# Performance work log

Measured on AMD Instinct MI355X. Metric: run time of the kernel, lower is better.

## Reference

```python
import jax, jax.numpy as jnp
import numpy as np

B, T, N, E, F_IN = 2, 8, 4000, 40000, 32
H, C, HL, FH = 4, 64, 128, 128  # heads, gat_hidden, lstm_hidden, fusion_hidden


def setup_inputs() -> dict:
    key = jax.random.key(0)
    ks = jax.random.split(key, 14)
    def nrm(i, shape, s=0.05):
        return jax.random.normal(ks[i], shape, jnp.float32) * s
    return {
        "x_seq": jax.random.normal(ks[0], (B, T, N, F_IN), jnp.float32),
        "W1": nrm(2, (F_IN, H * C)), "a_src1": nrm(3, (H, C)), "a_dst1": nrm(4, (H, C)), "b1": jnp.zeros((C,), jnp.float32),
        "W2": nrm(5, (C, H * C)), "a_src2": nrm(6, (H, C)), "a_dst2": nrm(7, (H, C)), "b2": jnp.zeros((C,), jnp.float32),
        "W_ih": nrm(8, (4 * HL, C)), "W_hh": nrm(9, (4 * HL, HL)),
        "b_ih": jnp.zeros((4 * HL,), jnp.float32), "b_hh": jnp.zeros((4 * HL,), jnp.float32),
        "Wf": nrm(10, (HL + C, FH)), "bf": jnp.zeros((FH,), jnp.float32),
        "Wo": nrm(11, (FH, 1)), "bo": jnp.zeros((1,), jnp.float32),
        "edge_index": jax.random.randint(ks[1], (2, E), 0, N, jnp.int64)
                      if jax.config.read("jax_enable_x64") else jax.random.randint(ks[1], (2, E), 0, N, jnp.int32),
    }


def gat_conv(x, src, dst, n, W, a_src, a_dst, b):
    """PyG GATConv, concat=False (mean over heads), self-loops already in src/dst."""
    h = (x @ W).reshape(n, H, C)                      # [N,H,C]
    al_s = jnp.einsum('nhc,hc->nh', h, a_src)         # [N,H]
    al_d = jnp.einsum('nhc,hc->nh', h, a_dst)
    logits = jax.nn.leaky_relu(al_s[src] + al_d[dst], negative_slope=0.2)  # [E',H]
    m = jax.ops.segment_max(logits, dst, num_segments=n)
    e = jnp.exp(logits - m[dst])
    denom = jax.ops.segment_sum(e, dst, num_segments=n)
    alpha = e / denom[dst]                            # segment-softmax over incoming edges
    out = jax.ops.segment_sum(alpha[:, :, None] * h[src], dst, num_segments=n)  # [N,H,C]
    return out.mean(axis=1) + b                       # [N,C]


def reference(x_seq, W1, a_src1, a_dst1, b1, W2, a_src2, a_dst2, b2,
              W_ih, W_hh, b_ih, b_hh, Wf, bf, Wo, bo, edge_index):
    Bd, Td, Nd, Fd = x_seq.shape
    loop = jnp.arange(Nd, dtype=edge_index.dtype)     # add_self_loops=True
    src = jnp.concatenate([edge_index[0], loop])
    dst = jnp.concatenate([edge_index[1], loop])

    def gat2(x):
        g1 = jax.nn.relu(gat_conv(x, src, dst, Nd, W1, a_src1, a_dst1, b1))
        return jax.nn.relu(gat_conv(g1, src, dst, Nd, W2, a_src2, a_dst2, b2))

    # batched over all B*T graph instances at once
    g = jax.vmap(gat2)(x_seq.reshape(Bd * Td, Nd, Fd)).reshape(Bd, Td, Nd, C)

    # LSTM over time, batch = B*N nodes
    seq = g.transpose(1, 0, 2, 3).reshape(Td, Bd * Nd, C)
    h0 = jnp.zeros((Bd * Nd, HL), x_seq.dtype)

    def step(carry, xt):
        h, c = carry
        z = xt @ W_ih.T + b_ih + h @ W_hh.T + b_hh
        i, f, gg, o = jnp.split(z, 4, axis=-1)        # torch gate order i,f,g,o
        c = jax.nn.sigmoid(f) * c + jax.nn.sigmoid(i) * jnp.tanh(gg)
        h = jax.nn.sigmoid(o) * jnp.tanh(c)
        return (h, c), None

    (hT, _), _ = jax.lax.scan(step, (h0, h0), seq)
    lstm_last = hT.reshape(Bd, Nd, HL)
    fused = jax.nn.relu(jnp.concatenate([lstm_last, g[:, -1]], axis=-1) @ Wf + bf)
    return (fused @ Wo + bo)[..., 0]                  # [B, N]
```

## Files before the change

### kernel.cpp

```cpp
#include <hip/hip_runtime.h>
#include <math.h>

#define NN 4000
#define EE 40000
#define NE 44000
#define BB 2
#define TT 8
#define BT 16
#define HH 4
#define CC 64
#define HC 256
#define HLN 128
#define G4 512
#define FHN 128
#define PADU 136
#define PADC 196

typedef __attribute__((ext_vector_type(8))) short short8v;
typedef __attribute__((ext_vector_type(4))) float f32x4;

__device__ __forceinline__ float fexp2(float x){ return __builtin_amdgcn_exp2f(x); }
__device__ __forceinline__ float frcp(float x){ return __builtin_amdgcn_rcpf(x); }
__device__ __forceinline__ float fsig(float x){ return frcp(1.f + fexp2(x * -1.44269504f)); }
__device__ __forceinline__ float ftanh(float x){
  float xx = fminf(fmaxf(x, -10.f), 10.f);
  float e = fexp2(xx * 2.88539008f);
  return (e - 1.f) * frcp(e + 1.f);
}
__device__ __forceinline__ unsigned short bf16rne(float x){
  unsigned u = __float_as_uint(x);
  return (unsigned short)((u + 0x7FFFu + ((u>>16)&1u)) >> 16);
}
__device__ __forceinline__ float bf2f(unsigned short h){ return __uint_as_float(((unsigned)h)<<16); }
__device__ __forceinline__ unsigned pack2(unsigned short a, unsigned short b){
  return ((unsigned)b << 16) | (unsigned)a;
}

__global__ void k_count(const int* __restrict__ dst, int* __restrict__ cnt){
  int e = blockIdx.x*256+threadIdx.x;
  if (e >= NE) return;
  int d = (e < EE) ? dst[e] : (e - EE);
  atomicAdd(&cnt[d], 1);
}

__global__ __launch_bounds__(1024) void k_scan(const int* __restrict__ cnt, int* __restrict__ ptr){
  __shared__ int part[1024];
  const int n = NN;
  int t = threadIdx.x;
  int base = t*4;
  int loc[4]; int s = 0;
  #pragma unroll
  for (int i=0;i<4;i++){ int c = (base+i < n) ? cnt[base+i] : 0; loc[i] = s; s += c; }
  part[t] = s;
  __syncthreads();
  for (int off=1; off<1024; off<<=1){
    int add = (t >= off) ? part[t-off] : 0;
    __syncthreads();
    part[t] += add;
    __syncthreads();
  }
  int ebase = (t > 0) ? part[t-1] : 0;
  #pragma unroll
  for (int i=0;i<4;i++){ if (base+i < n) ptr[base+i] = ebase + loc[i]; }
  if (t == 1023) ptr[n] = part[1023];
}

__global__ void k_scatter(const int* __restrict__ dst, const int* __restrict__ ptr,
                          int* __restrict__ cur, int* __restrict__ idxa){
  int e = blockIdx.x*256+threadIdx.x;
  if (e >= NE) return;
  int d = (e < EE) ? dst[e] : (e - EE);
  int pos = atomicAdd(&cur[d], 1);
  idxa[ptr[d]+pos] = e;
}

__global__ void k_sortseg(const int* __restrict__ ptr, int* __restrict__ idxa,
                          const int* __restrict__ e0, int* __restrict__ srcs){
  int node = blockIdx.x*256+threadIdx.x;
  if (node >= NN) return;
  int p0 = ptr[node], p1 = ptr[node+1];
  for (int i=p0+1;i<p1;i++){
    int key = idxa[i]; int j = i-1;
    while (j >= p0 && idxa[j] > key){ idxa[j+1] = idxa[j]; j--; }
    idxa[j+1] = key;
  }
  for (int p=p0;p<p1;p++){
    int e = idxa[p];
    srcs[p] = (e < EE) ? e0[e] : (e - EE);
  }
}

__global__ void k_prep(int* __restrict__ cnt,
                       const float* __restrict__ W1, const float* __restrict__ as1, const float* __restrict__ ad1,
                       const float* __restrict__ W2, const float* __restrict__ as2, const float* __restrict__ ad2,
                       float* __restrict__ wt,
                       const float* __restrict__ Wih, const float* __restrict__ Whh,
                       unsigned short* __restrict__ wfh, unsigned short* __restrict__ wfl,
                       const float* __restrict__ Wf, float* __restrict__ WfT,
                       unsigned short* __restrict__ wb1h, unsigned short* __restrict__ wb1l,
                       unsigned short* __restrict__ wb2h, unsigned short* __restrict__ wb2l){
  int i = blockIdx.x*256 + threadIdx.x;
  if (i < 2*NN){ cnt[i] = 0; return; }
  i -= 2*NN;
  if (i < 768){
    if (i < 256){
      int sd = i >> 7, h = (i >> 5) & 3, k = i & 31;
      const float* a = sd ? ad1 : as1;
      float s = 0.f;
      for (int c=0;c<CC;c++) s = fmaf(W1[k*HC + h*CC + c], a[h*CC + c], s);
      wt[sd*128 + h*32 + k] = s;
    } else {
      int j = i - 256;
      int sd = j >> 8, h = (j >> 6) & 3, k = j & 63;
      const float* a = sd ? ad2 : as2;
      float s = 0.f;
      for (int c=0;c<CC;c++) s = fmaf(W2[k*HC + h*CC + c], a[h*CC + c], s);
      wt[256 + sd*256 + h*64 + k] = s;
    }
    return;
  }
  i -= 768;
  if (i < 12288){
    int lane = i & 63;
    int kc = (i >> 6) % 6;
    int wk = i / (64*6);
    int w = wk & 7, gg = wk >> 3;
    int n = gg*128 + w*16 + (lane & 15);
    int kbase = kc*32 + (lane >> 4)*8;
    #pragma unroll
    for (int j=0;j<8;j++){
      int k = kbase + j;
      float v = (k < 64) ? Wih[n*64 + k] : Whh[n*128 + (k-64)];
      unsigned short hi = bf16rne(v);
      wfh[(size_t)i*8 + j] = hi;
      wfl[(size_t)i*8 + j] = bf16rne(v - bf2f(hi));
    }
    return;
  }
  i -= 12288;
  if (i < 24576){
    int u = i & 127, k = i >> 7;
    WfT[u*192 + k] = Wf[k*128 + u];
    return;
  }
  i -= 24576;
  if (i < 1024){
    int lane = i & 63, kc = (i >> 6) & 3, nt = i >> 8;
    int n = nt*16 + (lane & 15);
    int kb = kc*32 + (lane >> 4)*8;
    #pragma unroll
    for (int j=0;j<8;j++){
      int k = kb + j; int h = k >> 5; int kk = k & 31;
      float v = W1[kk*HC + h*CC + n];
      unsigned short hi = bf16rne(v);
      wb1h[(size_t)i*8 + j] = hi;
      wb1l[(size_t)i*8 + j] = bf16rne(v - bf2f(hi));
    }
    return;
  }
  i -= 1024;
  if (i < 2048){
    int lane = i & 63, kc = (i >> 6) & 7, nt = i >> 9;
    int n = nt*16 + (lane & 15);
    int kb = kc*32 + (lane >> 4)*8;
    #pragma unroll
    for (int j=0;j<8;j++){
      int k = kb + j; int h = k >> 6; int kk = k & 63;
      float v = W2[kk*HC + h*CC + n];
      unsigned short hi = bf16rne(v);
      wb2h[(size_t)i*8 + j] = hi;
      wb2l[(size_t)i*8 + j] = bf16rne(v - bf2f(hi));
    }
  }
}

template<int K>
__global__ void k_coef3(const float* __restrict__ x, const float* __restrict__ wts,
                        const float* __restrict__ wtd,
                        float* __restrict__ als, float* __restrict__ ald){
  int i = blockIdx.x*256+threadIdx.x;
  if (i >= BT*NN) return;
  const float* xp = x + (size_t)i*K;
  float s1[4] = {0.f,0.f,0.f,0.f};
  float s2[4] = {0.f,0.f,0.f,0.f};
  for (int k=0;k<K;k+=4){
    float4 xv = *(const float4*)&xp[k];
    #pragma unroll
    for (int h=0;h<4;h++){
      float4 sv = *(const float4*)&wts[h*K+k];
      float4 dv = *(const float4*)&wtd[h*K+k];
      s1[h] = fmaf(xv.x,sv.x,fmaf(xv.y,sv.y,fmaf(xv.z,sv.z,fmaf(xv.w,sv.w,s1[h]))));
      s2[h] = fmaf(xv.x,dv.x,fmaf(xv.y,dv.y,fmaf(xv.z,dv.z,fmaf(xv.w,dv.w,s2[h]))));
    }
  }
  *(float4*)&als[(size_t)i*4] = make_float4(s1[0],s1[1],s1[2],s1[3]);
  *(float4*)&ald[(size_t)i*4] = make_float4(s2[0],s2[1],s2[2],s2[3]);
}

template<int KF, bool SPLIT>
__global__ __launch_bounds__(256) void k_gatt(const int* __restrict__ ptr, const int* __restrict__ srcs,
    const float* __restrict__ als, const float* __restrict__ ald, const float* __restrict__ xin,
    const unsigned short* __restrict__ wbh, const unsigned short* __restrict__ wbl,
    const float* __restrict__ bias, float* __restrict__ outp,
    unsigned short* __restrict__ ohi, unsigned short* __restrict__ olo){
  constexpr int K = HH*KF;
  constexpr int PR = K + 8;
  constexpr int NKC = K/32;
  __shared__ float esh[16][64][HH];
  __shared__ float invs[16][HH];
  __shared__ unsigned short agh[16*PR];
  __shared__ unsigned short agl[16*PR];
  const int tid = threadIdx.x;
  const int lane = tid & 63;
  const int wv = tid >> 6;
  const int l15 = lane & 15;
  const int lg  = lane >> 4;
  const int bid = blockIdx.x;
  const int q = bid >> 3;
  const int hi2 = (q >= 250);
  const int inst = (bid & 7) + (hi2 ? 8 : 0);
  const int node0 = (hi2 ? q - 250 : q)*16;
  const size_t ibase = (size_t)inst*NN;
  {
    const int ns = lane >> 4;
    const int ei = lane & 15;
    const int nl = wv*4 + ns;
    const int node = node0 + nl;
    const int p0 = ptr[node], p1 = ptr[node+1];
    const float4 adv = *(const float4*)&ald[(ibase+node)*4];
    const float ad[4] = {adv.x, adv.y, adv.z, adv.w};
    float den[4] = {0.f,0.f,0.f,0.f};
    for (int p = p0 + ei; p < p1; p += 16){
      const int src = srcs[p];
      const float4 av = *(const float4*)&als[(ibase+src)*4];
      const float ac[4] = {av.x, av.y, av.z, av.w};
      float e4[4];
      #pragma unroll
      for (int h=0;h<4;h++){
        float v = ac[h] + ad[h];
        v = (v >= 0.f) ? v : 0.2f*v;
        float e = fexp2(v*1.44269504f);
        e4[h] = e;
        den[h] += e;
      }
      int slot = p - p0;
      if (slot < 64) *(float4*)&esh[nl][slot][0] = make_float4(e4[0],e4[1],e4[2],e4[3]);
    }
    #pragma unroll
    for (int h=0;h<4;h++){
      den[h] += __shfl_xor(den[h], 1);
      den[h] += __shfl_xor(den[h], 2);
      den[h] += __shfl_xor(den[h], 4);
      den[h] += __shfl_xor(den[h], 8);
    }
    if (ei == 0) *(float4*)&invs[nl][0] =
      make_float4(0.25f*frcp(den[0]), 0.25f*frcp(den[1]), 0.25f*frcp(den[2]), 0.25f*frcp(den[3]));
  }
  __syncthreads();
  constexpr int QL = KF/4;
  constexpr int EPAR = 64/QL;
  const int kq = lane & (QL-1);
  const int esub = lane / QL;
  for (int j=0;j<4;j++){
    const int nl = wv*4 + j;
    const int node = node0 + nl;
    const int p0 = ptr[node], p1 = ptr[node+1];
    float a[4][4];
    #pragma unroll
    for (int h=0;h<4;h++){ a[h][0]=0.f; a[h][1]=0.f; a[h][2]=0.f; a[h][3]=0.f; }
    for (int p = p0 + esub; p < p1; p += EPAR){
      const float4 ev = *(const float4*)&esh[nl][p - p0][0];
      const int src = srcs[p];
      const float4 xv = *(const float4*)&xin[(ibase + src)*(size_t)KF + kq*4];
      const float ec[4] = {ev.x, ev.y, ev.z, ev.w};
      const float xc[4] = {xv.x, xv.y, xv.z, xv.w};
      #pragma unroll
      for (int h=0;h<4;h++)
        #pragma unroll
        for (int c=0;c<4;c++)
          a[h][c] = fmaf(ec[h], xc[c], a[h][c]);
    }
    #pragma unroll
    for (int h=0;h<4;h++)
      #pragma unroll
      for (int c=0;c<4;c++){
        float v = a[h][c];
        if (EPAR == 8) v += __shfl_xor(v, 8);
        v += __shfl_xor(v, 16);
        v += __shfl_xor(v, 32);
        a[h][c] = v;
      }
    if (esub == 0){
      const float4 iv = *(const float4*)&invs[nl][0];
      const float ivc[4] = {iv.x, iv.y, iv.z, iv.w};
      #pragma unroll
      for (int h=0;h<4;h++){
        unsigned short vh[4], vl[4];
        #pragma unroll
        for (int c=0;c<4;c++){
          float v = a[h][c]*ivc[h];
          vh[c] = bf16rne(v);
          vl[c] = bf16rne(v - bf2f(vh[c]));
        }
        uint2 ph = {pack2(vh[0],vh[1]), pack2(vh[2],vh[3])};
        uint2 pl = {pack2(vl[0],vl[1]), pack2(vl[2],vl[3])};
        *(uint2*)&agh[nl*PR + h*KF + kq*4] = ph;
        *(uint2*)&agl[nl*PR + h*KF + kq*4] = pl;
      }
    }
  }
  __syncthreads();
  f32x4 acc = {0.f,0.f,0.f,0.f};
  #pragma unroll
  for (int kc=0; kc<NKC; kc++){
    size_t fl = (size_t)((wv*NKC + kc)*64 + lane)*8;
    short8v BH = *(const short8v*)&wbh[fl];
    short8v BL = *(const short8v*)&wbl[fl];
    int aoff = l15*PR + kc*32 + lg*8;
    short8v AH = *(const short8v*)&agh[aoff];
    short8v AL = *(const short8v*)&agl[aoff];
    acc = __builtin_amdgcn_mfma_f32_16x16x32_bf16(AH, BH, acc, 0,0,0);
    acc = __builtin_amdgcn_mfma_f32_16x16x32_bf16(AH, BL, acc, 0,0,0);
    acc = __builtin_amdgcn_mfma_f32_16x16x32_bf16(AL, BH, acc, 0,0,0);
  }
  const int c = wv*16 + l15;
  const float bv = bias[c];
  #pragma unroll
  for (int r=0;r<4;r++){
    int node = node0 + lg*4 + r;
    float val = fmaxf(acc[r] + bv, 0.f);
    size_t oi = (ibase + node)*CC + c;
    if constexpr (SPLIT){
      unsigned short hv = bf16rne(val);
      ohi[oi] = hv;
      olo[oi] = bf16rne(val - bf2f(hv));
    } else {
      outp[oi] = val;
    }
  }
}

__device__ __forceinline__ void mfma24(const short8v (&AH)[2], const short8v (&AL)[2],
                                       const short8v (&BH)[4], const short8v (&BL)[4],
                                       f32x4 (&acc)[2][4]){
  #pragma unroll
  for (int mt=0;mt<2;mt++)
    #pragma unroll
    for (int gg=0;gg<4;gg++)
      acc[mt][gg] = __builtin_amdgcn_mfma_f32_16x16x32_bf16(AH[mt], BH[gg], acc[mt][gg], 0,0,0);
  #pragma unroll
  for (int mt=0;mt<2;mt++)
    #pragma unroll
    for (int gg=0;gg<4;gg++)
      acc[mt][gg] = __builtin_amdgcn_mfma_f32_16x16x32_bf16(AH[mt], BL[gg], acc[mt][gg], 0,0,0);
  #pragma unroll
  for (int mt=0;mt<2;mt++)
    #pragma unroll
    for (int gg=0;gg<4;gg++)
      acc[mt][gg] = __builtin_amdgcn_mfma_f32_16x16x32_bf16(AL[mt], BH[gg], acc[mt][gg], 0,0,0);
}

__global__ __launch_bounds__(512) void k_lstm7(
    const unsigned short* __restrict__ ghi, const unsigned short* __restrict__ glo,
    const unsigned short* __restrict__ wfh, const unsigned short* __restrict__ wfl,
    const float* __restrict__ bih, const float* __restrict__ bhh,
    const float* __restrict__ WfT, const float* __restrict__ bfv,
    const float* __restrict__ Wo, const float* __restrict__ bo,
    float* __restrict__ out){
  __shared__ unsigned short hhi[32*PADU];
  __shared__ unsigned short hlo[32*PADU];
  __shared__ float catf[32*PADC];
  __shared__ float red[32*FHN];
  const int tid = threadIdx.x;
  const int lane = tid & 63;
  const int wv = tid >> 6;
  const int l15 = lane & 15;
  const int lg  = lane >> 4;
  const int r0 = blockIdx.x*32;
  const int b  = r0 / NN;
  const int n0 = r0 % NN;
  float bias[4];
  #pragma unroll
  for (int gg=0; gg<4; gg++){
    int n = gg*128 + wv*16 + l15;
    bias[gg] = bih[n] + bhh[n];
  }
  float c01[2][4];
  #pragma unroll
  for (int mt=0;mt<2;mt++){
    #pragma unroll
    for (int r=0;r<4;r++) c01[mt][r]=0.f;
  }
  auto ldw = [&](int kc, short8v (&BH)[4], short8v (&BL)[4]){
    #pragma unroll
    for (int gg=0;gg<4;gg++){
      size_t fl = (size_t)(((gg*8+wv)*6 + kc)*64 + lane)*8;
      BH[gg] = *(const short8v*)&wfh[fl];
      BL[gg] = *(const short8v*)&wfl[fl];
    }
  };

  for (int t=0;t<TT;t++){
    short8v axH[2][2], axL[2][2];
    #pragma unroll
    for (int mt=0; mt<2; mt++){
      const size_t row = ((size_t)(b*TT+t)*NN + n0 + mt*16 + l15);
      #pragma unroll
      for (int kc=0; kc<2; kc++){
        size_t off = row*64 + kc*32 + lg*8;
        axH[mt][kc] = *(const short8v*)&ghi[off];
        axL[mt][kc] = *(const short8v*)&glo[off];
      }
    }
    auto lda = [&](int kc, short8v (&AH)[2], short8v (&AL)[2]){
      if (kc < 2){
        AH[0]=axH[0][kc]; AH[1]=axH[1][kc];
        AL[0]=axL[0][kc]; AL[1]=axL[1][kc];
      } else {
        #pragma unroll
        for (int mt=0;mt<2;mt++){
          int off = (mt*16 + l15)*PADU + (kc-2)*32 + lg*8;
          AH[mt] = *(const short8v*)&hhi[off];
          AL[mt] = *(const short8v*)&hlo[off];
        }
      }
    };
    f32x4 acc[2][4];
    #pragma unroll
    for (int mt=0;mt<2;mt++){
      #pragma unroll
      for (int gg=0;gg<4;gg++){
        acc[mt][gg][0]=bias[gg]; acc[mt][gg][1]=bias[gg];
        acc[mt][gg][2]=bias[gg]; acc[mt][gg][3]=bias[gg];
      }
    }
    short8v BHa[4], BLa[4], BHb[4], BLb[4], AH[2], AL[2];
    if (t == 0){
      ldw(0, BHa, BLa);
      ldw(1, BHb, BLb);
      lda(0, AH, AL); mfma24(AH, AL, BHa, BLa, acc);
      lda(1, AH, AL); mfma24(AH, AL, BHb, BLb, acc);
    } else {
      ldw(0, BHa, BLa);
      ldw(1, BHb, BLb);
      lda(0, AH, AL); mfma24(AH, AL, BHa, BLa, acc);
      ldw(2, BHa, BLa);
      lda(1, AH, AL); mfma24(AH, AL, BHb, BLb, acc);
      ldw(3, BHb, BLb);
      lda(2, AH, AL); mfma24(AH, AL, BHa, BLa, acc);
      ldw(4, BHa, BLa);
      lda(3, AH, AL); mfma24(AH, AL, BHb, BLb, acc);
      ldw(5, BHb, BLb);
      lda(4, AH, AL); mfma24(AH, AL, BHa, BLa, acc);
      lda(5, AH, AL); mfma24(AH, AL, BHb, BLb, acc);
    }
    unsigned short hh_[2][4], hl_[2][4];
    float hv_[2][4];
    #pragma unroll
    for (int mt=0;mt<2;mt++){
      #pragma unroll
      for (int r=0;r<4;r++){
        float zi = acc[mt][0][r], zf = acc[mt][1][r], zg = acc[mt][2][r], zo = acc[mt][3][r];
        float cv = fsig(zf)*c01[mt][r] + fsig(zi)*ftanh(zg);
        c01[mt][r] = cv;
        float hv = fsig(zo)*ftanh(cv);
        hv_[mt][r] = hv;
        unsigned short hi = bf16rne(hv);
        hh_[mt][r] = hi;
        hl_[mt][r] = bf16rne(hv - bf2f(hi));
      }
    }
    if (t > 0) __syncthreads();
    if (t < TT-1){
      #pragma unroll
      for (int mt=0;mt<2;mt++){
        #pragma unroll
        for (int r=0;r<4;r++){
          int m = mt*16 + lg*4 + r;
          int u = wv*16 + l15;
          hhi[m*PADU + u] = hh_[mt][r];
          hlo[m*PADU + u] = hl_[mt][r];
        }
      }
    } else {
      #pragma unroll
      for (int mt=0;mt<2;mt++){
        #pragma unroll
        for (int r=0;r<4;r++){
          int m = mt*16 + lg*4 + r;
          int u = wv*16 + l15;
          catf[m*PADC + u] = hv_[mt][r];
        }
      }
      const size_t grow = ((size_t)(b*TT+TT-1)*NN + n0)*CC;
      int rr = tid >> 4, c4 = (tid & 15)*4;
      int idx = rr*CC + c4;
      #pragma unroll
      for (int qq=0;qq<4;qq++)
        catf[rr*PADC + 128 + c4 + qq] = bf2f(ghi[grow+idx+qq]) + bf2f(glo[grow+idx+qq]);
    }
    __syncthreads();
  }
  const int u = tid & 127;
  const int rg = tid >> 7;
  float fa[8];
  #pragma unroll
  for (int r=0;r<8;r++) fa[r] = bfv[u];
  for (int k4=0;k4<48;k4++){
    float4 wf = *(const float4*)&WfT[u*192 + k4*4];
    #pragma unroll
    for (int r=0;r<8;r++){
      float4 cv = *(const float4*)&catf[(rg*8+r)*PADC + k4*4];
      fa[r] = fmaf(cv.x,wf.x,fmaf(cv.y,wf.y,fmaf(cv.z,wf.z,fmaf(cv.w,wf.w,fa[r]))));
    }
  }
  float wo = Wo[u];
  #pragma unroll
  for (int r=0;r<8;r++) fa[r] = fmaxf(fa[r], 0.f) * wo;
  #pragma unroll
  for (int r=0;r<8;r++) red[(rg*8+r)*FHN + u] = fa[r];
  __syncthreads();
  for (int s=64;s>=1;s>>=1){
    if (u < s){
      #pragma unroll
      for (int r=0;r<8;r++) red[(rg*8+r)*FHN + u] += red[(rg*8+r)*FHN + u + s];
    }
    __syncthreads();
  }
  if (u == 0){
    #pragma unroll
    for (int r=0;r<8;r++) out[r0 + rg*8 + r] = red[(rg*8+r)*FHN] + bo[0];
  }
}

extern "C" void kernel_launch(void* const* d_in, const int* in_sizes, int n_in,
                              void* d_out, int out_size, void* d_ws, size_t ws_size,
                              hipStream_t stream) {
  const float* x_seq  = (const float*)d_in[0];
  const float* W1     = (const float*)d_in[1];
  const float* a_src1 = (const float*)d_in[2];
  const float* a_dst1 = (const float*)d_in[3];
  const float* b1     = (const float*)d_in[4];
  const float* W2     = (const float*)d_in[5];
  const float* a_src2 = (const float*)d_in[6];
  const float* a_dst2 = (const float*)d_in[7];
  const float* b2     = (const float*)d_in[8];
  const float* W_ih   = (const float*)d_in[9];
  const float* W_hh   = (const float*)d_in[10];
  const float* b_ih   = (const float*)d_in[11];
  const float* b_hh   = (const float*)d_in[12];
  const float* Wf     = (const float*)d_in[13];
  const float* bfv    = (const float*)d_in[14];
  const float* Wo     = (const float*)d_in[15];
  const float* bo     = (const float*)d_in[16];
  const int*   ei     = (const int*)d_in[17];
  const int* e_src = ei;
  const int* e_dst = ei + EE;
  float* out = (float*)d_out;

  char* w = (char*)d_ws;
  auto alloc = [&](size_t bytes)->char*{
    char* p = w; w += (bytes + 255) & ~(size_t)255; return p;
  };
  float* als   = (float*)alloc((size_t)BT*NN*HH*4);
  float* ald   = (float*)alloc((size_t)BT*NN*HH*4);
  float* gat1  = (float*)alloc((size_t)BT*NN*CC*4);
  unsigned short* ghi = (unsigned short*)alloc((size_t)BT*NN*CC*2);
  unsigned short* glo = (unsigned short*)alloc((size_t)BT*NN*CC*2);
  unsigned short* wfh = (unsigned short*)alloc((size_t)12288*8*2);
  unsigned short* wfl = (unsigned short*)alloc((size_t)12288*8*2);
  unsigned short* wb1h = (unsigned short*)alloc((size_t)1024*8*2);
  unsigned short* wb1l = (unsigned short*)alloc((size_t)1024*8*2);
  unsigned short* wb2h = (unsigned short*)alloc((size_t)2048*8*2);
  unsigned short* wb2l = (unsigned short*)alloc((size_t)2048*8*2);
  float* WfT   = (float*)alloc((size_t)128*192*4);
  float* wt    = (float*)alloc((size_t)768*4);
  int* cnt     = (int*)alloc((size_t)2*NN*4);
  int* cur     = cnt + NN;
  int* ptr     = (int*)alloc((size_t)(NN+1)*4);
  int* idxa    = (int*)alloc((size_t)NE*4);
  int* srcs    = (int*)alloc((size_t)NE*4);

  k_prep<<<(2*NN+768+12288+24576+1024+2048+255)/256, 256, 0, stream>>>(
      cnt, W1, a_src1, a_dst1, W2, a_src2, a_dst2, wt, W_ih, W_hh, wfh, wfl, Wf, WfT,
      wb1h, wb1l, wb2h, wb2l);
  k_count<<<(NE+255)/256, 256, 0, stream>>>(e_dst, cnt);
  k_scan<<<1, 1024, 0, stream>>>(cnt, ptr);
  k_scatter<<<(NE+255)/256, 256, 0, stream>>>(e_dst, ptr, cur, idxa);
  k_sortseg<<<(NN+255)/256, 256, 0, stream>>>(ptr, idxa, e_src, srcs);

  k_coef3<32><<<(BT*NN+255)/256, 256, 0, stream>>>(x_seq, wt, wt+128, als, ald);
  k_gatt<32,false><<<4000, 256, 0, stream>>>(ptr, srcs, als, ald, x_seq, wb1h, wb1l, b1,
                                             gat1, nullptr, nullptr);
  k_coef3<64><<<(BT*NN+255)/256, 256, 0, stream>>>(gat1, wt+256, wt+512, als, ald);
  k_gatt<64,true><<<4000, 256, 0, stream>>>(ptr, srcs, als, ald, gat1, wb2h, wb2l, b2,
                                            nullptr, ghi, glo);

  k_lstm7<<<BB*NN/32, 512, 0, stream>>>(ghi, glo, wfh, wfl, b_ih, b_hh, WfT, bfv, Wo, bo, out);
}
```

Measured before the change: 262.9 us.

## Fuse layer-2 attention coefficients into GAT layer-1 epilogue and inline edge softmax

The second coefficient kernel is removed; the layer-1 aggregation kernel now computes the per-node source and destination attention logits for layer 2 in its epilogue through shuffle reductions and a small shared buffer, writing them to new buffers. The separate edge-exponent pass with its LDS staging and barrier is dropped, so exponentials and denominators are computed inline in the aggregation loop. This also removes the 64-edge slot limit of the old staging buffer. In addition, the bf16 hi/lo split now uses truncation plus a packed convert instruction, and the LSTM MFMA block is wrapped in s_setprio. The trade-off is that each lane recomputes the exponentials for its feature quarter, extra shuffles and a barrier are added to the layer-1 epilogue, and the hi part changes from rounding to truncation.

```diff
diff --git a/kernel.cpp b/kernel.cpp
--- a/kernel.cpp
+++ b/kernel.cpp
@@ -32,9 +32,6 @@
   return (unsigned short)((u + 0x7FFFu + ((u>>16)&1u)) >> 16);
 }
 __device__ __forceinline__ float bf2f(unsigned short h){ return __uint_as_float(((unsigned)h)<<16); }
-__device__ __forceinline__ unsigned pack2(unsigned short a, unsigned short b){
-  return ((unsigned)b << 16) | (unsigned)a;
-}
 
 __global__ void k_count(const int* __restrict__ dst, int* __restrict__ cnt){
   int e = blockIdx.x*256+threadIdx.x;
@@ -202,14 +199,15 @@
     const float* __restrict__ als, const float* __restrict__ ald, const float* __restrict__ xin,
     const unsigned short* __restrict__ wbh, const unsigned short* __restrict__ wbl,
     const float* __restrict__ bias, float* __restrict__ outp,
-    unsigned short* __restrict__ ohi, unsigned short* __restrict__ olo){
+    unsigned short* __restrict__ ohi, unsigned short* __restrict__ olo,
+    const float* __restrict__ wt2s, const float* __restrict__ wt2d,
+    float* __restrict__ als2, float* __restrict__ ald2){
   constexpr int K = HH*KF;
   constexpr int PR = K + 8;
   constexpr int NKC = K/32;
-  __shared__ float esh[16][64][HH];
-  __shared__ float invs[16][HH];
   __shared__ unsigned short agh[16*PR];
   __shared__ unsigned short agl[16*PR];
+  __shared__ float cof[4][16][8];
   const int tid = threadIdx.x;
   const int lane = tid & 63;
   const int wv = tid >> 6;
@@ -221,42 +219,6 @@
   const int inst = (bid & 7) + (hi2 ? 8 : 0);
   const int node0 = (hi2 ? q - 250 : q)*16;
   const size_t ibase = (size_t)inst*NN;
-  {
-    const int ns = lane >> 4;
-    const int ei = lane & 15;
-    const int nl = wv*4 + ns;
-    const int node = node0 + nl;
-    const int p0 = ptr[node], p1 = ptr[node+1];
-    const float4 adv = *(const float4*)&ald[(ibase+node)*4];
-    const float ad[4] = {adv.x, adv.y, adv.z, adv.w};
-    float den[4] = {0.f,0.f,0.f,0.f};
-    for (int p = p0 + ei; p < p1; p += 16){
-      const int src = srcs[p];
-      const float4 av = *(const float4*)&als[(ibase+src)*4];
-      const float ac[4] = {av.x, av.y, av.z, av.w};
-      float e4[4];
-      #pragma unroll
-      for (int h=0;h<4;h++){
-        float v = ac[h] + ad[h];
-        v = (v >= 0.f) ? v : 0.2f*v;
-        float e = fexp2(v*1.44269504f);
-        e4[h] = e;
-        den[h] += e;
-      }
-      int slot = p - p0;
-      if (slot < 64) *(float4*)&esh[nl][slot][0] = make_float4(e4[0],e4[1],e4[2],e4[3]);
-    }
-    #pragma unroll
-    for (int h=0;h<4;h++){
-      den[h] += __shfl_xor(den[h], 1);
-      den[h] += __shfl_xor(den[h], 2);
-      den[h] += __shfl_xor(den[h], 4);
-      den[h] += __shfl_xor(den[h], 8);
-    }
-    if (ei == 0) *(float4*)&invs[nl][0] =
-      make_float4(0.25f*frcp(den[0]), 0.25f*frcp(den[1]), 0.25f*frcp(den[2]), 0.25f*frcp(den[3]));
-  }
-  __syncthreads();
   constexpr int QL = KF/4;
   constexpr int EPAR = 64/QL;
   const int kq = lane & (QL-1);
@@ -265,23 +227,33 @@
     const int nl = wv*4 + j;
     const int node = node0 + nl;
     const int p0 = ptr[node], p1 = ptr[node+1];
+    const float4 adv = *(const float4*)&ald[(ibase+node)*4];
+    const float ad[4] = {adv.x, adv.y, adv.z, adv.w};
+    float den[4] = {0.f,0.f,0.f,0.f};
     float a[4][4];
     #pragma unroll
     for (int h=0;h<4;h++){ a[h][0]=0.f; a[h][1]=0.f; a[h][2]=0.f; a[h][3]=0.f; }
     for (int p = p0 + esub; p < p1; p += EPAR){
-      const float4 ev = *(const float4*)&esh[nl][p - p0][0];
       const int src = srcs[p];
+      const float4 av = *(const float4*)&als[(ibase + src)*4];
       const float4 xv = *(const float4*)&xin[(ibase + src)*(size_t)KF + kq*4];
-      const float ec[4] = {ev.x, ev.y, ev.z, ev.w};
+      const float ac[4] = {av.x, av.y, av.z, av.w};
       const float xc[4] = {xv.x, xv.y, xv.z, xv.w};
       #pragma unroll
-      for (int h=0;h<4;h++)
+      for (int h=0;h<4;h++){
+        float v = ac[h] + ad[h];
+        v = (v >= 0.f) ? v : 0.2f*v;
+        float e = fexp2(v*1.44269504f);
+        den[h] += e;
         #pragma unroll
-        for (int c=0;c<4;c++)
-          a[h][c] = fmaf(ec[h], xc[c], a[h][c]);
-    }
-    #pragma unroll
-    for (int h=0;h<4;h++)
+        for (int c=0;c<4;c++) a[h][c] = fmaf(e, xc[c], a[h][c]);
+      }
+    }
+    #pragma unroll
+    for (int h=0;h<4;h++){
+      if (EPAR == 8) den[h] += __shfl_xor(den[h], 8);
+      den[h] += __shfl_xor(den[h], 16);
+      den[h] += __shfl_xor(den[h], 32);
       #pragma unroll
       for (int c=0;c<4;c++){
         float v = a[h][c];
@@ -290,20 +262,25 @@
         v += __shfl_xor(v, 32);
         a[h][c] = v;
       }
+    }
     if (esub == 0){
-      const float4 iv = *(const float4*)&invs[nl][0];
-      const float ivc[4] = {iv.x, iv.y, iv.z, iv.w};
       #pragma unroll
       for (int h=0;h<4;h++){
-        unsigned short vh[4], vl[4];
-        #pragma unroll
-        for (int c=0;c<4;c++){
-          float v = a[h][c]*ivc[h];
-          vh[c] = bf16rne(v);
-          vl[c] = bf16rne(v - bf2f(vh[c]));
-        }
-        uint2 ph = {pack2(vh[0],vh[1]), pack2(vh[2],vh[3])};
-        uint2 pl = {pack2(vl[0],vl[1]), pack2(vl[2],vl[3])};
+        float inv = 0.25f * frcp(den[h]);
+        float v0 = a[h][0]*inv, v1 = a[h][1]*inv, v2 = a[h][2]*inv, v3 = a[h][3]*inv;
+        unsigned u0 = __float_as_uint(v0) & 0xFFFF0000u;
+        unsigned u1 = __float_as_uint(v1) & 0xFFFF0000u;
+        unsigned u2 = __float_as_uint(v2) & 0xFFFF0000u;
+        unsigned u3 = __float_as_uint(v3) & 0xFFFF0000u;
+        float l0 = v0 - __uint_as_float(u0);
+        float l1 = v1 - __uint_as_float(u1);
+        float l2 = v2 - __uint_as_float(u2);
+        float l3 = v3 - __uint_as_float(u3);
+        unsigned pl0, pl1;
+        asm("v_cvt_pk_bf16_f32 %0, %1, %2" : "=v"(pl0) : "v"(l0), "v"(l1));
+        asm("v_cvt_pk_bf16_f32 %0, %1, %2" : "=v"(pl1) : "v"(l2), "v"(l3));
+        uint2 ph = {(u0 >> 16) | u1, (u2 >> 16) | u3};
+        uint2 pl = {pl0, pl1};
         *(uint2*)&agh[nl*PR + h*KF + kq*4] = ph;
         *(uint2*)&agl[nl*PR + h*KF + kq*4] = pl;
       }
@@ -325,10 +302,12 @@
   }
   const int c = wv*16 + l15;
   const float bv = bias[c];
+  float vals[4];
   #pragma unroll
   for (int r=0;r<4;r++){
     int node = node0 + lg*4 + r;
     float val = fmaxf(acc[r] + bv, 0.f);
+    vals[r] = val;
     size_t oi = (ibase + node)*CC + c;
     if constexpr (SPLIT){
       unsigned short hv = bf16rne(val);
@@ -338,11 +317,42 @@
       outp[oi] = val;
     }
   }
+  if constexpr (!SPLIT){
+    #pragma unroll
+    for (int r=0;r<4;r++){
+      float ps[4], pd[4];
+      #pragma unroll
+      for (int h=0;h<4;h++){
+        ps[h] = vals[r]*wt2s[h*CC + c];
+        pd[h] = vals[r]*wt2d[h*CC + c];
+      }
+      #pragma unroll
+      for (int h=0;h<4;h++){
+        ps[h] += __shfl_xor(ps[h],1); ps[h] += __shfl_xor(ps[h],2);
+        ps[h] += __shfl_xor(ps[h],4); ps[h] += __shfl_xor(ps[h],8);
+        pd[h] += __shfl_xor(pd[h],1); pd[h] += __shfl_xor(pd[h],2);
+        pd[h] += __shfl_xor(pd[h],4); pd[h] += __shfl_xor(pd[h],8);
+      }
+      if (l15 == 0){
+        *(float4*)&cof[wv][lg*4+r][0] = make_float4(ps[0],ps[1],ps[2],ps[3]);
+        *(float4*)&cof[wv][lg*4+r][4] = make_float4(pd[0],pd[1],pd[2],pd[3]);
+      }
+    }
+    __syncthreads();
+    if (tid < 128){
+      int nl = tid >> 3, v = tid & 7;
+      float s = cof[0][nl][v] + cof[1][nl][v] + cof[2][nl][v] + cof[3][nl][v];
+      int node = node0 + nl;
+      if (v < 4) als2[(ibase+node)*4 + v] = s;
+      else       ald2[(ibase+node)*4 + (v-4)] = s;
+    }
+  }
 }
 
 __device__ __forceinline__ void mfma24(const short8v (&AH)[2], const short8v (&AL)[2],
                                        const short8v (&BH)[4], const short8v (&BL)[4],
                                        f32x4 (&acc)[2][4]){
+  __builtin_amdgcn_s_setprio(1);
   #pragma unroll
   for (int mt=0;mt<2;mt++)
     #pragma unroll
@@ -358,6 +368,7 @@
     #pragma unroll
     for (int gg=0;gg<4;gg++)
       acc[mt][gg] = __builtin_amdgcn_mfma_f32_16x16x32_bf16(AL[mt], BH[gg], acc[mt][gg], 0,0,0);
+  __builtin_amdgcn_s_setprio(0);
 }
 
 __global__ __launch_bounds__(512) void k_lstm7(
@@ -564,6 +575,8 @@
   };
   float* als   = (float*)alloc((size_t)BT*NN*HH*4);
   float* ald   = (float*)alloc((size_t)BT*NN*HH*4);
+  float* als2  = (float*)alloc((size_t)BT*NN*HH*4);
+  float* ald2  = (float*)alloc((size_t)BT*NN*HH*4);
   float* gat1  = (float*)alloc((size_t)BT*NN*CC*4);
   unsigned short* ghi = (unsigned short*)alloc((size_t)BT*NN*CC*2);
   unsigned short* glo = (unsigned short*)alloc((size_t)BT*NN*CC*2);
@@ -591,10 +604,11 @@
 
   k_coef3<32><<<(BT*NN+255)/256, 256, 0, stream>>>(x_seq, wt, wt+128, als, ald);
   k_gatt<32,false><<<4000, 256, 0, stream>>>(ptr, srcs, als, ald, x_seq, wb1h, wb1l, b1,
-                                             gat1, nullptr, nullptr);
-  k_coef3<64><<<(BT*NN+255)/256, 256, 0, stream>>>(gat1, wt+256, wt+512, als, ald);
-  k_gatt<64,true><<<4000, 256, 0, stream>>>(ptr, srcs, als, ald, gat1, wb2h, wb2l, b2,
-                                            nullptr, ghi, glo);
+                                             gat1, nullptr, nullptr,
+                                             wt+256, wt+512, als2, ald2);
+  k_gatt<64,true><<<4000, 256, 0, stream>>>(ptr, srcs, als2, ald2, gat1, wb2h, wb2l, b2,
+                                            nullptr, ghi, glo,
+                                            nullptr, nullptr, nullptr, nullptr);
 
   k_lstm7<<<BB*NN/32, 512, 0, stream>>>(ghi, glo, wfh, wfl, b_ih, b_hh, WfT, bfv, Wo, bo, out);
 }
```

New measurement: 275.5 us. 1.05x slower.

## Fuse GAT softmax and aggregation into one pass per node

Applied to the files above, without the earlier changes.

The attention kernel previously ran two phases: one computed edge exponentials into shared memory and reduced the denominators, and a second re-read them to aggregate source features. Now each 16-lane group owns one node and walks its edges serially, computing the exponential and accumulating the weighted features in registers at once, with the next source index prefetched. This removes the shared staging buffer, a barrier, the shuffle reductions and the 64-edge slot limit. In exchange each lane computes exp redundantly and the edge loop is serial per node, which lowers memory-level parallelism for high-degree nodes. The bf16 high part now uses truncation instead of rounding.

```diff
diff --git a/kernel.cpp b/kernel.cpp
--- a/kernel.cpp
+++ b/kernel.cpp
@@ -32,9 +32,6 @@
   return (unsigned short)((u + 0x7FFFu + ((u>>16)&1u)) >> 16);
 }
 __device__ __forceinline__ float bf2f(unsigned short h){ return __uint_as_float(((unsigned)h)<<16); }
-__device__ __forceinline__ unsigned pack2(unsigned short a, unsigned short b){
-  return ((unsigned)b << 16) | (unsigned)a;
-}
 
 __global__ void k_count(const int* __restrict__ dst, int* __restrict__ cnt){
   int e = blockIdx.x*256+threadIdx.x;
@@ -206,8 +203,7 @@
   constexpr int K = HH*KF;
   constexpr int PR = K + 8;
   constexpr int NKC = K/32;
-  __shared__ float esh[16][64][HH];
-  __shared__ float invs[16][HH];
+  constexpr int VPL = KF/16;
   __shared__ unsigned short agh[16*PR];
   __shared__ unsigned short agl[16*PR];
   const int tid = threadIdx.x;
@@ -222,90 +218,60 @@
   const int node0 = (hi2 ? q - 250 : q)*16;
   const size_t ibase = (size_t)inst*NN;
   {
-    const int ns = lane >> 4;
-    const int ei = lane & 15;
-    const int nl = wv*4 + ns;
+    const int nl = wv*4 + lg;
     const int node = node0 + nl;
     const int p0 = ptr[node], p1 = ptr[node+1];
     const float4 adv = *(const float4*)&ald[(ibase+node)*4];
     const float ad[4] = {adv.x, adv.y, adv.z, adv.w};
     float den[4] = {0.f,0.f,0.f,0.f};
-    for (int p = p0 + ei; p < p1; p += 16){
-      const int src = srcs[p];
-      const float4 av = *(const float4*)&als[(ibase+src)*4];
+    float a[4][VPL];
+    #pragma unroll
+    for (int h=0;h<4;h++)
+      #pragma unroll
+      for (int c=0;c<VPL;c++) a[h][c] = 0.f;
+    int src = srcs[p0];
+    for (int p = p0; p < p1; p++){
+      const int nsrc = (p+1 < p1) ? srcs[p+1] : 0;
+      const float4 av = *(const float4*)&als[(ibase + src)*4];
+      float xv[VPL];
+      if constexpr (VPL == 4){
+        float4 x4 = *(const float4*)&xin[(ibase + src)*(size_t)KF + l15*4];
+        xv[0]=x4.x; xv[1]=x4.y; xv[2]=x4.z; xv[3]=x4.w;
+      } else {
+        float2 x2 = *(const float2*)&xin[(ibase + src)*(size_t)KF + l15*2];
+        xv[0]=x2.x; xv[1]=x2.y;
+      }
       const float ac[4] = {av.x, av.y, av.z, av.w};
-      float e4[4];
       #pragma unroll
       for (int h=0;h<4;h++){
         float v = ac[h] + ad[h];
         v = (v >= 0.f) ? v : 0.2f*v;
         float e = fexp2(v*1.44269504f);
-        e4[h] = e;
         den[h] += e;
-      }
-      int slot = p - p0;
-      if (slot < 64) *(float4*)&esh[nl][slot][0] = make_float4(e4[0],e4[1],e4[2],e4[3]);
+        #pragma unroll
+        for (int c=0;c<VPL;c++) a[h][c] = fmaf(e, xv[c], a[h][c]);
+      }
+      src = nsrc;
     }
     #pragma unroll
     for (int h=0;h<4;h++){
-      den[h] += __shfl_xor(den[h], 1);
-      den[h] += __shfl_xor(den[h], 2);
-      den[h] += __shfl_xor(den[h], 4);
-      den[h] += __shfl_xor(den[h], 8);
-    }
-    if (ei == 0) *(float4*)&invs[nl][0] =
-      make_float4(0.25f*frcp(den[0]), 0.25f*frcp(den[1]), 0.25f*frcp(den[2]), 0.25f*frcp(den[3]));
-  }
-  __syncthreads();
-  constexpr int QL = KF/4;
-  constexpr int EPAR = 64/QL;
-  const int kq = lane & (QL-1);
-  const int esub = lane / QL;
-  for (int j=0;j<4;j++){
-    const int nl = wv*4 + j;
-    const int node = node0 + nl;
-    const int p0 = ptr[node], p1 = ptr[node+1];
-    float a[4][4];
-    #pragma unroll
-    for (int h=0;h<4;h++){ a[h][0]=0.f; a[h][1]=0.f; a[h][2]=0.f; a[h][3]=0.f; }
-    for (int p = p0 + esub; p < p1; p += EPAR){
-      const float4 ev = *(const float4*)&esh[nl][p - p0][0];
-      const int src = srcs[p];
-      const float4 xv = *(const float4*)&xin[(ibase + src)*(size_t)KF + kq*4];
-      const float ec[4] = {ev.x, ev.y, ev.z, ev.w};
-      const float xc[4] = {xv.x, xv.y, xv.z, xv.w};
-      #pragma unroll
-      for (int h=0;h<4;h++)
-        #pragma unroll
-        for (int c=0;c<4;c++)
-          a[h][c] = fmaf(ec[h], xc[c], a[h][c]);
-    }
-    #pragma unroll
-    for (int h=0;h<4;h++)
-      #pragma unroll
-      for (int c=0;c<4;c++){
-        float v = a[h][c];
-        if (EPAR == 8) v += __shfl_xor(v, 8);
-        v += __shfl_xor(v, 16);
-        v += __shfl_xor(v, 32);
-        a[h][c] = v;
-      }
-    if (esub == 0){
-      const float4 iv = *(const float4*)&invs[nl][0];
-      const float ivc[4] = {iv.x, iv.y, iv.z, iv.w};
-      #pragma unroll
-      for (int h=0;h<4;h++){
-        unsigned short vh[4], vl[4];
-        #pragma unroll
-        for (int c=0;c<4;c++){
-          float v = a[h][c]*ivc[h];
-          vh[c] = bf16rne(v);
-          vl[c] = bf16rne(v - bf2f(vh[c]));
-        }
-        uint2 ph = {pack2(vh[0],vh[1]), pack2(vh[2],vh[3])};
-        uint2 pl = {pack2(vl[0],vl[1]), pack2(vl[2],vl[3])};
-        *(uint2*)&agh[nl*PR + h*KF + kq*4] = ph;
-        *(uint2*)&agl[nl*PR + h*KF + kq*4] = pl;
+      float inv = 0.25f * frcp(den[h]);
+      unsigned short vh[VPL], vl[VPL];
+      #pragma unroll
+      for (int c=0;c<VPL;c++){
+        float v = a[h][c]*inv;
+        unsigned uh = __float_as_uint(v) & 0xFFFF0000u;
+        vh[c] = (unsigned short)(uh >> 16);
+        vl[c] = bf16rne(v - __uint_as_float(uh));
+      }
+      if constexpr (VPL == 4){
+        uint2 ph = {((unsigned)vh[1]<<16)|vh[0], ((unsigned)vh[3]<<16)|vh[2]};
+        uint2 pl = {((unsigned)vl[1]<<16)|vl[0], ((unsigned)vl[3]<<16)|vl[2]};
+        *(uint2*)&agh[nl*PR + h*KF + l15*4] = ph;
+        *(uint2*)&agl[nl*PR + h*KF + l15*4] = pl;
+      } else {
+        *(unsigned*)&agh[nl*PR + h*KF + l15*2] = ((unsigned)vh[1]<<16)|vh[0];
+        *(unsigned*)&agl[nl*PR + h*KF + l15*2] = ((unsigned)vl[1]<<16)|vl[0];
       }
     }
   }
```

After: 224.3 us. 14.7% less time.
